# Optimization experiments

Measured on AMD Instinct MI355X. Metric: run time of the kernel, lower is better.

The kernel has to match this reference:

```python
import jax, jax.numpy as jnp
import numpy as np

B, M, E, R = 4, 72, 24, 552          # docs, mentions/doc, entities/doc, pairs/doc
L, H, A = 1024, 1024, 16             # seq_len, hidden (LUKE-large), attn heads
EMB, BLK, OUT, NC = 768, 64, 768, 97 # embed_size, block_size, out_embed_size, num_class


def setup_inputs() -> dict:
    key = jax.random.key(0)
    ks = jax.random.split(key, 12)
    s = 0.02  # weight scale to keep tanh unsaturated
    return {
        "seq_lhs": jax.random.normal(ks[0], (B, L, H), jnp.float32),
        "ent_lhs": jax.random.normal(ks[1], (B, M, H), jnp.float32),
        "ent_to_seq_attn": jax.random.uniform(ks[2], (B, A, M, L), jnp.float32),
        "entity_id_labels": jax.random.randint(ks[3], (B, M), 0, E, jnp.int32),
        "hts": jax.random.randint(ks[4], (B, R, 2), 0, E, jnp.int32),
        "W_head": jax.random.normal(ks[5], (2 * H, EMB), jnp.float32) * s,
        "b_head": jnp.zeros((EMB,), jnp.float32),
        "W_tail": jax.random.normal(ks[6], (2 * H, EMB), jnp.float32) * s,
        "b_tail": jnp.zeros((EMB,), jnp.float32),
        "W_bil": jax.random.normal(ks[7], (EMB * BLK, OUT), jnp.float32) * s,
        "b_bil": jnp.zeros((OUT,), jnp.float32),
        "W_cls": jax.random.normal(ks[8], (OUT, NC), jnp.float32) * s,
        "b_cls": jnp.zeros((NC,), jnp.float32),
        "W_bin": jax.random.normal(ks[9], (OUT, 1), jnp.float32) * s,
        "b_bin": jnp.zeros((1,), jnp.float32),
    }


def _hrt_pool(seq_lhs, ent_lhs, ent_to_seq_attn, entity_id_labels, hts):
    # global segment id: doc_i * E + entity_label  -> [B*M]
    seg = (jnp.arange(B, dtype=entity_id_labels.dtype)[:, None] * E
           + entity_id_labels).reshape(-1)
    NSEG = B * E

    # --- entity embedding: logsumexp over mentions of each entity (0 if empty) ---
    x = ent_lhs.reshape(B * M, H)
    mx = jax.ops.segment_max(x, seg, num_segments=NSEG)          # -inf for empty
    mx_safe = jnp.where(jnp.isfinite(mx), mx, 0.0)
    ssum = jax.ops.segment_sum(jnp.exp(x - mx_safe[seg]), seg, num_segments=NSEG)
    cnt = jax.ops.segment_sum(jnp.ones((B * M,), x.dtype), seg, num_segments=NSEG)
    ent_emb = jnp.where(cnt[:, None] > 0, jnp.log(ssum) + mx_safe, 0.0)
    ent_emb = ent_emb.reshape(B, E, H)

    # --- entity-to-seq attention: mean over mentions (0 if empty) ---
    a = ent_to_seq_attn.transpose(0, 2, 1, 3).reshape(B * M, A, L)
    asum = jax.ops.segment_sum(a, seg, num_segments=NSEG)
    amean = jnp.where(cnt[:, None, None] > 0,
                      asum / jnp.maximum(cnt, 1.0)[:, None, None], 0.0)
    amean = amean.reshape(B, E, A, L)

    # --- gather head/tail per pair ---
    bidx = jnp.arange(B)[:, None]
    hs = ent_emb[bidx, hts[:, :, 0]]       # [B,R,H]
    ts = ent_emb[bidx, hts[:, :, 1]]
    ha = amean[bidx, hts[:, :, 0]]         # [B,R,A,L]
    ta = amean[bidx, hts[:, :, 1]]

    ht_attn = (ha * ta).mean(axis=2)       # [B,R,L] mean over heads
    ht_attn = ht_attn / (ht_attn.sum(axis=-1, keepdims=True) + 1e-5)
    rel = jnp.einsum('bld,brl->brd', seq_lhs, ht_attn)  # [B,R,H]
    return hs, ts, rel


def reference(seq_lhs, ent_lhs, ent_to_seq_attn, entity_id_labels, hts,
              W_head, b_head, W_tail, b_tail, W_bil, b_bil,
              W_cls, b_cls, W_bin, b_bin):
    hs, ts, rel = _hrt_pool(seq_lhs, ent_lhs, ent_to_seq_attn,
                            entity_id_labels, hts)
    N = B * R
    hs = jnp.tanh(jnp.concatenate([hs, rel], -1).reshape(N, 2 * H) @ W_head + b_head)
    ts = jnp.tanh(jnp.concatenate([ts, rel], -1).reshape(N, 2 * H) @ W_tail + b_tail)

    K = EMB // BLK
    b1 = hs.reshape(N, K, BLK)
    b2 = ts.reshape(N, K, BLK)
    bl = (b1[:, :, :, None] * b2[:, :, None, :]).reshape(N, EMB * BLK)
    embeds = bl @ W_bil + b_bil                    # [N, OUT]
    class_logits = embeds @ W_cls + b_cls          # [N, NC]
    binary_logits = embeds @ W_bin + b_bin         # [N, 1]
    return embeds, class_logits, binary_logits
```

## Files before the change

kernel.cpp:

```cpp
#include <hip/hip_runtime.h>
#include <hip/hip_bf16.h>
#include <math.h>
#include <stdint.h>

#define B_ 4
#define M_ 72
#define E_ 24
#define R_ 552
#define L_ 1024
#define H_ 1024
#define A_ 16
#define EMB_ 768
#define BLK_ 64
#define OUT_ 768
#define NC_ 97
#define N_ (B_*R_)
#define NPAD_ 2304
#define K2H_ (2*H_)
#define KB_ (EMB_/BLK_)
#define KTOT_ (EMB_*BLK_)
#define SLICE2_ 524288

typedef short s16x8 __attribute__((ext_vector_type(8)));
typedef float f32x4 __attribute__((ext_vector_type(4)));
typedef uint32_t u32x4 __attribute__((ext_vector_type(4)));

__device__ __forceinline__ uint32_t pkbf16(float lo, float hi) {
    uint32_t r;
    asm("v_cvt_pk_bf16_f32 %0, %1, %2" : "=v"(r) : "v"(lo), "v"(hi));
    return r;
}
__device__ __forceinline__ unsigned short f2bf(float f) {
    uint32_t u = __builtin_bit_cast(uint32_t, f);
    uint32_t r = (u + 0x7fffu + ((u >> 16) & 1u)) >> 16;
    return (unsigned short)r;
}
__device__ __forceinline__ float bff(unsigned short u) {
    return __builtin_bit_cast(float, (uint32_t)u << 16);
}
__device__ __forceinline__ void gload_lds16(const void* g, void* l) {
    __builtin_amdgcn_global_load_lds(
        (const __attribute__((address_space(1))) unsigned int*)g,
        (__attribute__((address_space(3))) unsigned int*)l, 16, 0, 0);
}

__global__ void k_pool(const float* __restrict__ ent_lhs,
                       const float* __restrict__ attn,
                       const int*   __restrict__ labels,
                       unsigned short* __restrict__ ent_bf,
                       unsigned short* __restrict__ amean_bf)
{
    int b = blockIdx.x / E_;
    int e = blockIdx.x % E_;
    __shared__ int mlist[M_];
    __shared__ int mcount;
    if (threadIdx.x == 0) {
        int c = 0;
        for (int m = 0; m < M_; ++m)
            if (labels[b*M_ + m] == e) mlist[c++] = m;
        mcount = c;
    }
    __syncthreads();
    int cnt = mcount;

    for (int h = threadIdx.x; h < H_; h += blockDim.x) {
        float out = 0.f;
        if (cnt > 0) {
            float mx = -INFINITY;
            for (int q = 0; q < cnt; ++q)
                mx = fmaxf(mx, ent_lhs[(size_t)(b*M_ + mlist[q])*H_ + h]);
            float s = 0.f;
            for (int q = 0; q < cnt; ++q)
                s += expf(ent_lhs[(size_t)(b*M_ + mlist[q])*H_ + h] - mx);
            out = logf(s) + mx;
        }
        ent_bf[(size_t)(b*E_ + e)*H_ + h] = f2bf(out);
    }

    float inv = (cnt > 0) ? (1.f / (float)cnt) : 0.f;
    for (int c4 = threadIdx.x; c4 < A_*(L_/4); c4 += blockDim.x) {
        int a = c4 / (L_/4), l4 = c4 % (L_/4);
        float sx = 0.f, sy = 0.f, sz = 0.f, sw = 0.f;
        for (int q = 0; q < cnt; ++q) {
            float4 v = *(const float4*)(attn + ((size_t)(b*A_ + a)*M_ + mlist[q])*L_ + l4*4);
            sx += v.x; sy += v.y; sz += v.z; sw += v.w;
        }
        ushort4 o;
        o.x = f2bf(sx*inv); o.y = f2bf(sy*inv); o.z = f2bf(sz*inv); o.w = f2bf(sw*inv);
        *(ushort4*)(amean_bf + ((size_t)(b*E_ + e)*A_ + a)*L_ + l4*4) = o;
    }
}

__global__ void k_htattn(const unsigned short* __restrict__ amean_bf,
                         const int* __restrict__ hts,
                         unsigned short* __restrict__ htw_bf)
{
    int br = blockIdx.x;
    int b  = br / R_;
    int hh = hts[br*2 + 0], tt = hts[br*2 + 1];
    const unsigned short* pa = amean_bf + (size_t)(b*E_ + hh)*A_*L_;
    const unsigned short* pb = amean_bf + (size_t)(b*E_ + tt)*A_*L_;

    int l0 = threadIdx.x * 4;
    float v[4] = {0.f, 0.f, 0.f, 0.f};
    for (int a = 0; a < A_; ++a) {
        ushort4 ua = *(const ushort4*)(pa + (size_t)a*L_ + l0);
        ushort4 ub = *(const ushort4*)(pb + (size_t)a*L_ + l0);
        v[0] += bff(ua.x)*bff(ub.x); v[1] += bff(ua.y)*bff(ub.y);
        v[2] += bff(ua.z)*bff(ub.z); v[3] += bff(ua.w)*bff(ub.w);
    }
    float part = (v[0]+v[1]+v[2]+v[3]) * 0.0625f;
    __shared__ float red[256];
    red[threadIdx.x] = part;
    __syncthreads();
    for (int st = 128; st > 0; st >>= 1) {
        if (threadIdx.x < st) red[threadIdx.x] += red[threadIdx.x + st];
        __syncthreads();
    }
    float norm = 0.0625f / (red[0] + 1e-5f);
    unsigned short* po = htw_bf + (size_t)br*L_ + l0;
    po[0] = f2bf(v[0]*norm); po[1] = f2bf(v[1]*norm);
    po[2] = f2bf(v[2]*norm); po[3] = f2bf(v[3]*norm);
}

__global__ void k_transcvt(const float* __restrict__ W, unsigned short* __restrict__ Wt,
                           int K, int O)
{
    const float* src = W + (size_t)blockIdx.z*K*O;
    unsigned short* dst = Wt + (size_t)blockIdx.z*K*O;
    __shared__ unsigned short t[64][72];
    int k0 = blockIdx.x * 64, o0 = blockIdx.y * 64;
    #pragma unroll
    for (int p = 0; p < 16; ++p) {
        int idx = p*256 + threadIdx.x;
        int r = idx >> 6, c = idx & 63;
        t[c][r] = f2bf(src[(size_t)(k0 + r)*O + o0 + c]);
    }
    __syncthreads();
    #pragma unroll
    for (int p = 0; p < 16; ++p) {
        int idx = p*256 + threadIdx.x;
        int r = idx >> 6, c = idx & 63;
        dst[(size_t)(o0 + r)*K + k0 + c] = t[r][c];
    }
}

__global__ void k_cvtW2(const float* __restrict__ W, unsigned short* __restrict__ W2)
{
    __shared__ unsigned short t[64][72];
    int k0 = blockIdx.x * 64, o0 = blockIdx.y * 64;
    #pragma unroll
    for (int p = 0; p < 16; ++p) {
        int idx = p*256 + threadIdx.x;
        int r = idx >> 6, c = idx & 63;
        t[c][r] = f2bf(W[(size_t)(k0 + r)*OUT_ + o0 + c]);
    }
    __syncthreads();
    int kb = k0 >> 12;
    int i  = (k0 >> 6) & 63;
    int ob = o0 >> 7;
    int wc = (o0 >> 6) & 1;
    unsigned short* base = W2 + (size_t)(kb*6 + ob)*SLICE2_ + i*8192 + wc*4096;
    #pragma unroll
    for (int p = 0; p < 16; ++p) {
        int lin = p*256 + threadIdx.x;
        int e = lin & 7;
        int lane = (lin >> 3) & 63;
        int f = lin >> 9;
        int jh = f >> 2, ofl = f & 3;
        int j = (jh*4 + (lane >> 4))*8 + e;
        int o_local = ofl*16 + (lane & 15);
        base[f*512 + lane*8 + e] = t[o_local][j];
    }
}

__global__ void k_init(const float* __restrict__ b_head, const float* __restrict__ b_tail,
                       const float* __restrict__ b_bil,
                       const float* __restrict__ Wc, const float* __restrict__ Wbn,
                       float* __restrict__ pacc, float* __restrict__ embeds,
                       unsigned short* __restrict__ WcatT)
{
    int idx = blockIdx.x * 256 + threadIdx.x;
    if (idx < 2*NPAD_*OUT_) {
        const float* bb = (idx < NPAD_*OUT_) ? b_head : b_tail;
        pacc[idx] = bb[idx % OUT_];
    } else if (idx < 2*NPAD_*OUT_ + N_*OUT_) {
        int j = idx - 2*NPAD_*OUT_;
        embeds[j] = b_bil[j % OUT_];
    } else {
        int j = idx - 2*NPAD_*OUT_ - N_*OUT_;
        if (j < 256*768) {
            int o = j / 768, k = j % 768;
            float v = 0.f;
            if (o < NC_) v = Wc[(size_t)k*NC_ + o];
            else if (o == NC_) v = Wbn[k];
            WcatT[j] = f2bf(v);
        }
    }
}

__global__ __launch_bounds__(256, 2)
void k_rel_mfma(const unsigned short* __restrict__ htw,
                const unsigned short* __restrict__ seqT,
                unsigned short* __restrict__ rel_bf)
{
    int bid = blockIdx.x;
    int ot = bid & 7;
    int rest = bid >> 3;
    int mt = rest % 5;
    int b  = rest / 5;
    int m0 = mt*128, o0 = ot*128;
    int tid = threadIdx.x, lane = tid & 63, wid = tid >> 6;
    int wr = wid >> 1, wc = wid & 1;
    __shared__ __align__(16) unsigned short a_s[128*64];
    __shared__ __align__(16) unsigned short b_s[128*64];
    const unsigned short* Ab = htw + (size_t)b*R_*L_;
    const unsigned short* Bb = seqT + (size_t)b*H_*L_;

    u32x4 aR[4], bR[4];
    auto loadA = [&](int st) {
        #pragma unroll
        for (int q = 0; q < 4; ++q) {
            int slot = q*256 + tid;
            int r = slot >> 3, s = slot & 7;
            int ar = m0 + r; if (ar > R_-1) ar = R_-1;
            aR[q] = *(const u32x4*)(Ab + (size_t)ar*L_ + st*64 + s*8);
        }
    };
    auto loadB = [&](int st) {
        #pragma unroll
        for (int q = 0; q < 4; ++q) {
            int slot = q*256 + tid;
            int o = slot >> 3, s = slot & 7;
            bR[q] = *(const u32x4*)(Bb + (size_t)(o0+o)*L_ + st*64 + s*8);
        }
    };

    f32x4 acc[4][4];
    const f32x4 zz = {0.f,0.f,0.f,0.f};
    #pragma unroll
    for (int mf = 0; mf < 4; ++mf)
        #pragma unroll
        for (int of = 0; of < 4; ++of) acc[mf][of] = zz;

    loadA(0); loadB(0);
    for (int st = 0; st < 16; ++st) {
        __syncthreads();
        #pragma unroll
        for (int q = 0; q < 4; ++q) {
            int slot = q*256 + tid; int r = slot >> 3, s = slot & 7;
            *(u32x4*)((char*)a_s + r*128 + ((s ^ (r & 7)) << 4)) = aR[q];
        }
        #pragma unroll
        for (int q = 0; q < 4; ++q) {
            int slot = q*256 + tid; int o = slot >> 3, s = slot & 7;
            *(u32x4*)((char*)b_s + o*128 + ((s ^ (o & 7)) << 4)) = bR[q];
        }
        __syncthreads();
        if (st < 15) { loadA(st+1); loadB(st+1); }
        #pragma unroll
        for (int kh = 0; kh < 2; ++kh) {
            s16x8 af[4];
            #pragma unroll
            for (int mf = 0; mf < 4; ++mf) {
                int r = wr*64 + mf*16 + (lane & 15);
                int s = kh*4 + (lane >> 4);
                af[mf] = *(const s16x8*)((const char*)a_s + r*128 + ((s ^ (r & 7)) << 4));
            }
            #pragma unroll
            for (int of = 0; of < 4; ++of) {
                int ol = wc*64 + of*16 + (lane & 15);
                int s = kh*4 + (lane >> 4);
                s16x8 bfr = *(const s16x8*)((const char*)b_s + ol*128 + ((s ^ (ol & 7)) << 4));
                #pragma unroll
                for (int mf = 0; mf < 4; ++mf)
                    acc[mf][of] = __builtin_amdgcn_mfma_f32_16x16x32_bf16(
                        af[mf], bfr, acc[mf][of], 0, 0, 0);
            }
        }
    }
    #pragma unroll
    for (int mf = 0; mf < 4; ++mf)
        #pragma unroll
        for (int of = 0; of < 4; ++of) {
            int col = o0 + wc*64 + of*16 + (lane & 15);
            #pragma unroll
            for (int rr = 0; rr < 4; ++rr) {
                int row = m0 + wr*64 + mf*16 + (lane >> 4)*4 + rr;
                if (row < R_)
                    rel_bf[((size_t)b*R_ + row)*H_ + col] = f2bf(acc[mf][of][rr]);
            }
        }
}

__global__ __launch_bounds__(256, 2)
void k_proj_mfma(const unsigned short* __restrict__ ent_bf,
                 const unsigned short* __restrict__ rel_bf,
                 const int* __restrict__ hts,
                 const unsigned short* __restrict__ Wph,
                 const unsigned short* __restrict__ Wpt,
                 float* __restrict__ pacc)
{
    int bid = blockIdx.x;
    int kq = bid & 3;
    int rest = bid >> 2;
    int ob = rest % 3;  rest /= 3;
    int mb = rest % 18;
    int which = rest / 18;
    int m0 = mb * 128, o0 = ob * 256;
    const unsigned short* Wp = which ? Wpt : Wph;
    float* out = pacc + (size_t)which*NPAD_*OUT_;
    int tid = threadIdx.x, lane = tid & 63, wid = tid >> 6;
    int wr = wid >> 1, wc = wid & 1;
    __shared__ __align__(16) unsigned short a_s[128*64];
    __shared__ __align__(16) unsigned short b_s[256*64];

    bool enthalf = (kq < 2);
    const unsigned short* abase[4];
    #pragma unroll
    for (int q = 0; q < 4; ++q) {
        int slot = q*256 + tid;
        int r = slot >> 3;
        int n = m0 + r;
        int nn = (n < N_) ? n : (N_ - 1);
        if (enthalf) {
            int bb = nn / R_;
            abase[q] = ent_bf + (size_t)(bb*E_ + hts[nn*2 + which])*H_ + kq*512;
        } else {
            abase[q] = rel_bf + (size_t)nn*H_ + (kq - 2)*512;
        }
    }
    u32x4 aR[4], bR[8];
    auto loadA = [&](int st) {
        #pragma unroll
        for (int q = 0; q < 4; ++q) {
            int s = (q*256 + tid) & 7;
            aR[q] = *(const u32x4*)(abase[q] + st*64 + s*8);
        }
    };
    auto loadB = [&](int st) {
        #pragma unroll
        for (int q = 0; q < 8; ++q) {
            int slot = q*256 + tid;
            int o = slot >> 3, s = slot & 7;
            bR[q] = *(const u32x4*)(Wp + (size_t)(o0+o)*K2H_ + kq*512 + st*64 + s*8);
        }
    };

    f32x4 acc[4][8];
    const f32x4 zz = {0.f,0.f,0.f,0.f};
    #pragma unroll
    for (int mf = 0; mf < 4; ++mf)
        #pragma unroll
        for (int of = 0; of < 8; ++of) acc[mf][of] = zz;

    loadA(0); loadB(0);
    for (int st = 0; st < 8; ++st) {
        __syncthreads();
        #pragma unroll
        for (int q = 0; q < 4; ++q) {
            int slot = q*256 + tid; int r = slot >> 3, s = slot & 7;
            *(u32x4*)((char*)a_s + r*128 + ((s ^ (r & 7)) << 4)) = aR[q];
        }
        #pragma unroll
        for (int q = 0; q < 8; ++q) {
            int slot = q*256 + tid; int o = slot >> 3, s = slot & 7;
            *(u32x4*)((char*)b_s + o*128 + ((s ^ (o & 7)) << 4)) = bR[q];
        }
        __syncthreads();
        if (st < 7) { loadA(st+1); loadB(st+1); }
        #pragma unroll
        for (int kh = 0; kh < 2; ++kh) {
            s16x8 af[4];
            #pragma unroll
            for (int mf = 0; mf < 4; ++mf) {
                int r = wr*64 + mf*16 + (lane & 15);
                int s = kh*4 + (lane >> 4);
                af[mf] = *(const s16x8*)((const char*)a_s + r*128 + ((s ^ (r & 7)) << 4));
            }
            #pragma unroll
            for (int of = 0; of < 8; ++of) {
                int ol = wc*128 + of*16 + (lane & 15);
                int s = kh*4 + (lane >> 4);
                s16x8 bfr = *(const s16x8*)((const char*)b_s + ol*128 + ((s ^ (ol & 7)) << 4));
                #pragma unroll
                for (int mf = 0; mf < 4; ++mf)
                    acc[mf][of] = __builtin_amdgcn_mfma_f32_16x16x32_bf16(
                        af[mf], bfr, acc[mf][of], 0, 0, 0);
            }
        }
    }
    #pragma unroll
    for (int mf = 0; mf < 4; ++mf)
        #pragma unroll
        for (int of = 0; of < 8; ++of) {
            int col = o0 + wc*128 + of*16 + (lane & 15);
            #pragma unroll
            for (int rr = 0; rr < 4; ++rr) {
                int row = m0 + wr*64 + mf*16 + (lane >> 4)*4 + rr;
                atomicAdd(&out[(size_t)row*OUT_ + col], acc[mf][of][rr]);
            }
        }
}

__global__ void k_tanhcvt(const float* __restrict__ pacc,
                          unsigned short* __restrict__ hsp,
                          unsigned short* __restrict__ tsp)
{
    int idx = blockIdx.x * 256 + threadIdx.x;
    if (idx < NPAD_*OUT_) {
        hsp[idx] = f2bf(tanhf(pacc[idx]));
        tsp[idx] = f2bf(tanhf(pacc[NPAD_*OUT_ + idx]));
    }
}

__global__ __launch_bounds__(256, 2)
void k_bilinear_mfma(const unsigned short* __restrict__ hsp,
                     const unsigned short* __restrict__ tsp,
                     const unsigned short* __restrict__ W2,
                     float* __restrict__ embeds)
{
    int bid = blockIdx.x;
    int x = bid & 7, rest = bid >> 3;
    int g = rest / 18, mb = rest % 18;
    int s = g*8 + x;
    int kb = s / 6, ob = s % 6;
    int m0 = mb * 128;
    int tid = threadIdx.x, lane = tid & 63, wid = tid >> 6;
    int wr = wid >> 1, wc = wid & 1;

    __shared__ __align__(16) unsigned short hs_s[128*64];
    __shared__ __align__(16) unsigned short ts_s[128*64];

    #pragma unroll
    for (int q = 0; q < 4; ++q) {
        int slot = q*256 + tid;
        int r = slot >> 3, s7 = slot & 7;
        int gg = s7 ^ (r & 7);
        size_t srcoff = (size_t)(m0 + r)*EMB_ + kb*64 + (gg << 3);
        gload_lds16(hsp + srcoff, (char*)hs_s + (q*4096 + wid*1024));
        gload_lds16(tsp + srcoff, (char*)ts_s + (q*4096 + wid*1024));
    }
    __syncthreads();

    float tsf[4][2][8];
    #pragma unroll
    for (int mf = 0; mf < 4; ++mf) {
        int r = wr*64 + mf*16 + (lane & 15);
        #pragma unroll
        for (int jh = 0; jh < 2; ++jh) {
            int s8 = jh*4 + (lane >> 4);
            u32x4 tv = *(const u32x4*)((const char*)ts_s + r*128 + ((s8 ^ (r & 7)) << 4));
            #pragma unroll
            for (int p = 0; p < 4; ++p) {
                tsf[mf][jh][2*p]   = __builtin_bit_cast(float, tv[p] << 16);
                tsf[mf][jh][2*p+1] = __builtin_bit_cast(float, tv[p] & 0xffff0000u);
            }
        }
    }

    const unsigned short* Wsl = W2 + (size_t)s * SLICE2_ + wc*4096 + lane*8;

    f32x4 acc[4][4];
    const f32x4 zz = {0.f, 0.f, 0.f, 0.f};
    #pragma unroll
    for (int mf = 0; mf < 4; ++mf)
        #pragma unroll
        for (int of = 0; of < 4; ++of) acc[mf][of] = zz;

    u32x4 bA[8], bB[8];
    auto loadB = [&](int i, u32x4 (&buf)[8]) {
        const unsigned short* src = Wsl + (size_t)i*8192;
        #pragma unroll
        for (int f = 0; f < 8; ++f)
            buf[f] = *(const u32x4*)(src + f*512);
    };
    auto compute = [&](int i, u32x4 (&buf)[8]) {
        float hsf[4];
        #pragma unroll
        for (int mf = 0; mf < 4; ++mf) {
            int r = wr*64 + mf*16 + (lane & 15);
            int hb = r*128 + ((((i >> 3)) ^ (r & 7)) << 4) + (i & 7)*2;
            hsf[mf] = bff(*(const unsigned short*)((const char*)hs_s + hb));
        }
        #pragma unroll
        for (int jh = 0; jh < 2; ++jh) {
            s16x8 afr[4];
            #pragma unroll
            for (int mf = 0; mf < 4; ++mf) {
                u32x4 a;
                #pragma unroll
                for (int p = 0; p < 4; ++p)
                    a[p] = pkbf16(hsf[mf]*tsf[mf][jh][2*p], hsf[mf]*tsf[mf][jh][2*p+1]);
                afr[mf] = __builtin_bit_cast(s16x8, a);
            }
            #pragma unroll
            for (int of = 0; of < 4; ++of) {
                s16x8 bfr = __builtin_bit_cast(s16x8, buf[jh*4 + of]);
                #pragma unroll
                for (int mf = 0; mf < 4; ++mf)
                    acc[mf][of] = __builtin_amdgcn_mfma_f32_16x16x32_bf16(
                        afr[mf], bfr, acc[mf][of], 0, 0, 0);
            }
        }
    };

    loadB(0, bA);
    for (int i2 = 0; i2 < 32; ++i2) {
        loadB(2*i2 + 1, bB);
        compute(2*i2, bA);
        if (i2 < 31) loadB(2*i2 + 2, bA);
        compute(2*i2 + 1, bB);
    }

    #pragma unroll
    for (int mf = 0; mf < 4; ++mf) {
        #pragma unroll
        for (int of = 0; of < 4; ++of) {
            int col = ob*128 + wc*64 + of*16 + (lane & 15);
            #pragma unroll
            for (int rr = 0; rr < 4; ++rr) {
                int row = wr*64 + mf*16 + (lane >> 4)*4 + rr;
                int n = m0 + row;
                if (n < N_)
                    atomicAdd(&embeds[(size_t)n*OUT_ + col], acc[mf][of][rr]);
            }
        }
    }
}

__global__ __launch_bounds__(256, 2)
void k_logits_mfma(const float* __restrict__ embeds,
                   const unsigned short* __restrict__ WcatT,
                   const float* __restrict__ bc, const float* __restrict__ bbn,
                   float* __restrict__ cls, float* __restrict__ bin)
{
    int m0 = blockIdx.x * 128;
    int tid = threadIdx.x, lane = tid & 63, wid = tid >> 6;
    int wr = wid >> 1, wc = wid & 1;
    __shared__ __align__(16) unsigned short a_s[128*64];
    __shared__ __align__(16) unsigned short b_s[256*64];

    u32x4 aR[4], bR[8];
    auto loadA = [&](int st) {
        #pragma unroll
        for (int q = 0; q < 4; ++q) {
            int slot = q*256 + tid;
            int r = slot >> 3, s = slot & 7;
            int ar = m0 + r; if (ar > N_-1) ar = N_-1;
            const float* src = embeds + (size_t)ar*OUT_ + st*64 + s*8;
            float4 v0 = *(const float4*)(src);
            float4 v1 = *(const float4*)(src + 4);
            u32x4 a;
            a[0] = pkbf16(v0.x, v0.y); a[1] = pkbf16(v0.z, v0.w);
            a[2] = pkbf16(v1.x, v1.y); a[3] = pkbf16(v1.z, v1.w);
            aR[q] = a;
        }
    };
    auto loadB = [&](int st) {
        #pragma unroll
        for (int q = 0; q < 8; ++q) {
            int slot = q*256 + tid;
            int o = slot >> 3, s = slot & 7;
            bR[q] = *(const u32x4*)(WcatT + (size_t)o*OUT_ + st*64 + s*8);
        }
    };

    f32x4 acc[4][8];
    const f32x4 zz = {0.f,0.f,0.f,0.f};
    #pragma unroll
    for (int mf = 0; mf < 4; ++mf)
        #pragma unroll
        for (int of = 0; of < 8; ++of) acc[mf][of] = zz;

    loadA(0); loadB(0);
    for (int st = 0; st < 12; ++st) {
        __syncthreads();
        #pragma unroll
        for (int q = 0; q < 4; ++q) {
            int slot = q*256 + tid; int r = slot >> 3, s = slot & 7;
            *(u32x4*)((char*)a_s + r*128 + ((s ^ (r & 7)) << 4)) = aR[q];
        }
        #pragma unroll
        for (int q = 0; q < 8; ++q) {
            int slot = q*256 + tid; int o = slot >> 3, s = slot & 7;
            *(u32x4*)((char*)b_s + o*128 + ((s ^ (o & 7)) << 4)) = bR[q];
        }
        __syncthreads();
        if (st < 11) { loadA(st+1); loadB(st+1); }
        #pragma unroll
        for (int kh = 0; kh < 2; ++kh) {
            s16x8 af[4];
            #pragma unroll
            for (int mf = 0; mf < 4; ++mf) {
                int r = wr*64 + mf*16 + (lane & 15);
                int s = kh*4 + (lane >> 4);
                af[mf] = *(const s16x8*)((const char*)a_s + r*128 + ((s ^ (r & 7)) << 4));
            }
            #pragma unroll
            for (int of = 0; of < 8; ++of) {
                int ol = wc*128 + of*16 + (lane & 15);
                int s = kh*4 + (lane >> 4);
                s16x8 bfr = *(const s16x8*)((const char*)b_s + ol*128 + ((s ^ (ol & 7)) << 4));
                #pragma unroll
                for (int mf = 0; mf < 4; ++mf)
                    acc[mf][of] = __builtin_amdgcn_mfma_f32_16x16x32_bf16(
                        af[mf], bfr, acc[mf][of], 0, 0, 0);
            }
        }
    }
    #pragma unroll
    for (int mf = 0; mf < 4; ++mf)
        #pragma unroll
        for (int of = 0; of < 8; ++of) {
            int col = wc*128 + of*16 + (lane & 15);
            if (col <= NC_) {
                #pragma unroll
                for (int rr = 0; rr < 4; ++rr) {
                    int row = m0 + wr*64 + mf*16 + (lane >> 4)*4 + rr;
                    if (row < N_) {
                        float v = acc[mf][of][rr];
                        if (col < NC_) cls[(size_t)row*NC_ + col] = v + bc[col];
                        else           bin[row] = v + bbn[0];
                    }
                }
            }
        }
}

extern "C" void kernel_launch(void* const* d_in, const int* in_sizes, int n_in,
                              void* d_out, int out_size, void* d_ws, size_t ws_size,
                              hipStream_t stream) {
    const float* seq_lhs = (const float*)d_in[0];
    const float* ent_lhs = (const float*)d_in[1];
    const float* attn    = (const float*)d_in[2];
    const int*   labels  = (const int*)d_in[3];
    const int*   hts     = (const int*)d_in[4];
    const float* W_head  = (const float*)d_in[5];
    const float* b_head  = (const float*)d_in[6];
    const float* W_tail  = (const float*)d_in[7];
    const float* b_tail  = (const float*)d_in[8];
    const float* W_bil   = (const float*)d_in[9];
    const float* b_bil   = (const float*)d_in[10];
    const float* W_cls   = (const float*)d_in[11];
    const float* b_cls   = (const float*)d_in[12];
    const float* W_bin   = (const float*)d_in[13];
    const float* b_bin   = (const float*)d_in[14];

    float* out_embeds = (float*)d_out;
    float* out_cls    = out_embeds + (size_t)N_*OUT_;
    float* out_bin    = out_cls + (size_t)N_*NC_;

    float* ws = (float*)d_ws;
    size_t off = 0;
    unsigned short* ent_bf   = (unsigned short*)(ws + off); off += (size_t)B_*E_*H_/2;
    float* pacc = ws + off;
    unsigned short* amean_bf = (unsigned short*)(ws + off); off += (size_t)B_*E_*A_*L_/2;
    unsigned short* htw_bf   = (unsigned short*)(ws + off); off += (size_t)B_*R_*L_/2;
    unsigned short* seqT     = (unsigned short*)(ws + off); off += (size_t)B_*H_*L_/2;
    unsigned short* rel_bf   = (unsigned short*)(ws + off); off += (size_t)N_*H_/2;
    unsigned short* hsp      = (unsigned short*)(ws + off); off += (size_t)NPAD_*EMB_/2;
    unsigned short* tsp      = (unsigned short*)(ws + off); off += (size_t)NPAD_*EMB_/2;
    unsigned short* W2       = (unsigned short*)(ws + off); off += (size_t)OUT_*KTOT_/2;
    unsigned short* Wph      = (unsigned short*)(ws + off); off += (size_t)OUT_*K2H_/2;
    unsigned short* Wpt      = (unsigned short*)(ws + off); off += (size_t)OUT_*K2H_/2;
    unsigned short* WcatT    = (unsigned short*)(ws + off); off += (size_t)256*768/2;

    k_cvtW2<<<dim3(KTOT_/64, OUT_/64), 256, 0, stream>>>(W_bil, W2);
    k_transcvt<<<dim3(K2H_/64, OUT_/64, 1), 256, 0, stream>>>(W_head, Wph, K2H_, OUT_);
    k_transcvt<<<dim3(K2H_/64, OUT_/64, 1), 256, 0, stream>>>(W_tail, Wpt, K2H_, OUT_);
    k_transcvt<<<dim3(L_/64, H_/64, B_), 256, 0, stream>>>(seq_lhs, seqT, L_, H_);

    k_pool<<<B_*E_, 256, 0, stream>>>(ent_lhs, attn, labels, ent_bf, amean_bf);
    k_htattn<<<B_*R_, 256, 0, stream>>>(amean_bf, hts, htw_bf);
    k_rel_mfma<<<160, 256, 0, stream>>>(htw_bf, seqT, rel_bf);

    int init_elems = 2*NPAD_*OUT_ + N_*OUT_ + 256*768;
    k_init<<<(init_elems + 255)/256, 256, 0, stream>>>(b_head, b_tail, b_bil,
                                                       W_cls, W_bin,
                                                       pacc, out_embeds, WcatT);
    k_proj_mfma<<<2*18*3*4, 256, 0, stream>>>(ent_bf, rel_bf, hts, Wph, Wpt, pacc);
    k_tanhcvt<<<(NPAD_*OUT_ + 255)/256, 256, 0, stream>>>(pacc, hsp, tsp);

    k_bilinear_mfma<<<1296, 256, 0, stream>>>(hsp, tsp, W2, out_embeds);

    k_logits_mfma<<<18, 256, 0, stream>>>(out_embeds, WcatT, b_cls, b_bin,
                                          out_cls, out_bin);
}
```

Baseline: 460.0 us.

## Reshape bilinear MFMA tile to 64 rows by 256 columns with repacked weights

The bilinear GEMM tile changes from 128 rows x 128 output columns to 64 rows x 256 output columns per block. The W2 bf16 repack layout changes to match, with each k-block split into 3 column slices instead of 6. Each block now recomputes fewer hs*ts products per B fragment and streams a wider weight slice. The k-loop covers the jh halves as separate steps. The grid grows to 1440 blocks, with some blocks exiting early from the rounded-up grouping, and each block does more iterations.

Result: slower. 495.9 us (+7.8%).

```diff
diff --git a/kernel.cpp b/kernel.cpp
--- a/kernel.cpp
+++ b/kernel.cpp
@@ -19,7 +19,7 @@
 #define K2H_ (2*H_)
 #define KB_ (EMB_/BLK_)
 #define KTOT_ (EMB_*BLK_)
-#define SLICE2_ 524288
+#define SLICE_ 1048576
 
 typedef short s16x8 __attribute__((ext_vector_type(8)));
 typedef float f32x4 __attribute__((ext_vector_type(4)));
@@ -158,16 +158,18 @@
     __syncthreads();
     int kb = k0 >> 12;
     int i  = (k0 >> 6) & 63;
-    int ob = o0 >> 7;
-    int wc = (o0 >> 6) & 1;
-    unsigned short* base = W2 + (size_t)(kb*6 + ob)*SLICE2_ + i*8192 + wc*4096;
+    int ob = o0 >> 8;
+    int wc = (o0 >> 7) & 1;
+    int ofb = (o0 >> 4) & 7;
+    unsigned short* base = W2 + (size_t)(kb*3 + ob)*SLICE_ + i*16384 + wc*8192;
     #pragma unroll
     for (int p = 0; p < 16; ++p) {
         int lin = p*256 + threadIdx.x;
         int e = lin & 7;
         int lane = (lin >> 3) & 63;
-        int f = lin >> 9;
-        int jh = f >> 2, ofl = f & 3;
+        int fl = lin >> 9;
+        int jh = fl >> 2, ofl = fl & 3;
+        int f = jh*8 + ofb + ofl;
         int j = (jh*4 + (lane >> 4))*8 + e;
         int o_local = ofl*16 + (lane & 15);
         base[f*512 + lane*8 + e] = t[o_local][j];
@@ -422,18 +424,19 @@
 {
     int bid = blockIdx.x;
     int x = bid & 7, rest = bid >> 3;
-    int g = rest / 18, mb = rest % 18;
+    int g = rest / 36, mb = rest % 36;
     int s = g*8 + x;
-    int kb = s / 6, ob = s % 6;
-    int m0 = mb * 128;
+    if (s >= 36) return;
+    int kb = s / 3, ob = s % 3;
+    int m0 = mb * 64;
     int tid = threadIdx.x, lane = tid & 63, wid = tid >> 6;
     int wr = wid >> 1, wc = wid & 1;
 
-    __shared__ __align__(16) unsigned short hs_s[128*64];
-    __shared__ __align__(16) unsigned short ts_s[128*64];
-
-    #pragma unroll
-    for (int q = 0; q < 4; ++q) {
+    __shared__ __align__(16) unsigned short hs_s[64*64];
+    __shared__ __align__(16) unsigned short ts_s[64*64];
+
+    #pragma unroll
+    for (int q = 0; q < 2; ++q) {
         int slot = q*256 + tid;
         int r = slot >> 3, s7 = slot & 7;
         int gg = s7 ^ (r & 7);
@@ -443,10 +446,10 @@
     }
     __syncthreads();
 
-    float tsf[4][2][8];
-    #pragma unroll
-    for (int mf = 0; mf < 4; ++mf) {
-        int r = wr*64 + mf*16 + (lane & 15);
+    float tsf[2][2][8];
+    #pragma unroll
+    for (int mf = 0; mf < 2; ++mf) {
+        int r = wr*32 + mf*16 + (lane & 15);
         #pragma unroll
         for (int jh = 0; jh < 2; ++jh) {
             int s8 = jh*4 + (lane >> 4);
@@ -459,68 +462,62 @@
         }
     }
 
-    const unsigned short* Wsl = W2 + (size_t)s * SLICE2_ + wc*4096 + lane*8;
-
-    f32x4 acc[4][4];
+    const unsigned short* Wsl = W2 + (size_t)s * SLICE_ + wc*8192 + lane*8;
+
+    f32x4 acc[2][8];
     const f32x4 zz = {0.f, 0.f, 0.f, 0.f};
     #pragma unroll
-    for (int mf = 0; mf < 4; ++mf)
-        #pragma unroll
-        for (int of = 0; of < 4; ++of) acc[mf][of] = zz;
+    for (int mf = 0; mf < 2; ++mf)
+        #pragma unroll
+        for (int of = 0; of < 8; ++of) acc[mf][of] = zz;
 
     u32x4 bA[8], bB[8];
-    auto loadB = [&](int i, u32x4 (&buf)[8]) {
-        const unsigned short* src = Wsl + (size_t)i*8192;
+    auto loadU = [&](int u, u32x4 (&buf)[8]) {
+        const unsigned short* src = Wsl + (size_t)(u >> 1)*16384 + (u & 1)*4096;
         #pragma unroll
         for (int f = 0; f < 8; ++f)
             buf[f] = *(const u32x4*)(src + f*512);
     };
-    auto compute = [&](int i, u32x4 (&buf)[8]) {
-        float hsf[4];
-        #pragma unroll
-        for (int mf = 0; mf < 4; ++mf) {
-            int r = wr*64 + mf*16 + (lane & 15);
+    auto compute = [&](int u, u32x4 (&buf)[8]) {
+        int i = u >> 1, jh = u & 1;
+        s16x8 afr[2];
+        #pragma unroll
+        for (int mf = 0; mf < 2; ++mf) {
+            int r = wr*32 + mf*16 + (lane & 15);
             int hb = r*128 + ((((i >> 3)) ^ (r & 7)) << 4) + (i & 7)*2;
-            hsf[mf] = bff(*(const unsigned short*)((const char*)hs_s + hb));
-        }
-        #pragma unroll
-        for (int jh = 0; jh < 2; ++jh) {
-            s16x8 afr[4];
-            #pragma unroll
-            for (int mf = 0; mf < 4; ++mf) {
-                u32x4 a;
-                #pragma unroll
-                for (int p = 0; p < 4; ++p)
-                    a[p] = pkbf16(hsf[mf]*tsf[mf][jh][2*p], hsf[mf]*tsf[mf][jh][2*p+1]);
-                afr[mf] = __builtin_bit_cast(s16x8, a);
-            }
-            #pragma unroll
-            for (int of = 0; of < 4; ++of) {
-                s16x8 bfr = __builtin_bit_cast(s16x8, buf[jh*4 + of]);
-                #pragma unroll
-                for (int mf = 0; mf < 4; ++mf)
-                    acc[mf][of] = __builtin_amdgcn_mfma_f32_16x16x32_bf16(
-                        afr[mf], bfr, acc[mf][of], 0, 0, 0);
-            }
-        }
-    };
-
-    loadB(0, bA);
-    for (int i2 = 0; i2 < 32; ++i2) {
-        loadB(2*i2 + 1, bB);
-        compute(2*i2, bA);
-        if (i2 < 31) loadB(2*i2 + 2, bA);
-        compute(2*i2 + 1, bB);
-    }
-
-    #pragma unroll
-    for (int mf = 0; mf < 4; ++mf) {
-        #pragma unroll
-        for (int of = 0; of < 4; ++of) {
-            int col = ob*128 + wc*64 + of*16 + (lane & 15);
+            float hsf = bff(*(const unsigned short*)((const char*)hs_s + hb));
+            u32x4 a;
+            #pragma unroll
+            for (int p = 0; p < 4; ++p)
+                a[p] = pkbf16(hsf*tsf[mf][jh][2*p], hsf*tsf[mf][jh][2*p+1]);
+            afr[mf] = __builtin_bit_cast(s16x8, a);
+        }
+        #pragma unroll
+        for (int of = 0; of < 8; ++of) {
+            s16x8 bfr = __builtin_bit_cast(s16x8, buf[of]);
+            #pragma unroll
+            for (int mf = 0; mf < 2; ++mf)
+                acc[mf][of] = __builtin_amdgcn_mfma_f32_16x16x32_bf16(
+                    afr[mf], bfr, acc[mf][of], 0, 0, 0);
+        }
+    };
+
+    loadU(0, bA);
+    for (int u2 = 0; u2 < 64; ++u2) {
+        loadU(2*u2 + 1, bB);
+        compute(2*u2, bA);
+        if (u2 < 63) loadU(2*u2 + 2, bA);
+        compute(2*u2 + 1, bB);
+    }
+
+    #pragma unroll
+    for (int mf = 0; mf < 2; ++mf) {
+        #pragma unroll
+        for (int of = 0; of < 8; ++of) {
+            int col = ob*256 + wc*128 + of*16 + (lane & 15);
             #pragma unroll
             for (int rr = 0; rr < 4; ++rr) {
-                int row = wr*64 + mf*16 + (lane >> 4)*4 + rr;
+                int row = wr*32 + mf*16 + (lane >> 4)*4 + rr;
                 int n = m0 + row;
                 if (n < N_)
                     atomicAdd(&embeds[(size_t)n*OUT_ + col], acc[mf][of][rr]);
@@ -682,7 +679,7 @@
     k_proj_mfma<<<2*18*3*4, 256, 0, stream>>>(ent_bf, rel_bf, hts, Wph, Wpt, pacc);
     k_tanhcvt<<<(NPAD_*OUT_ + 255)/256, 256, 0, stream>>>(pacc, hsp, tsp);
 
-    k_bilinear_mfma<<<1296, 256, 0, stream>>>(hsp, tsp, W2, out_embeds);
+    k_bilinear_mfma<<<1440, 256, 0, stream>>>(hsp, tsp, W2, out_embeds);
 
     k_logits_mfma<<<18, 256, 0, stream>>>(out_embeds, WcatT, b_cls, b_bin,
                                           out_cls, out_bin);
```
